# Performance work log

Hardware: AMD Instinct MI355X
Metric: run time of the kernel (lower is better)

The kernel has to match this reference:

```python
import jax, jax.numpy as jnp
import numpy as np

B, N, E = 4, 2048, 512
H, DK, DV = 8, 64, 64
QKV_OUT = H * (2 * DK + DV)  # 1536


def setup_inputs() -> dict:
    key = jax.random.key(0)
    ks = jax.random.split(key, 5)
    s_in = 1.0 / np.sqrt(E)
    s_o = 1.0 / np.sqrt(H * DV)
    x = jax.random.normal(ks[0], (B, N, E), dtype=jnp.float32)
    W_qkv = jax.random.uniform(ks[1], (E, QKV_OUT), jnp.float32, -s_in, s_in)
    b_qkv = jax.random.uniform(ks[2], (QKV_OUT,), jnp.float32, -s_in, s_in)
    W_o = jax.random.uniform(ks[3], (H * DV, E), jnp.float32, -s_o, s_o)
    b_o = jax.random.uniform(ks[4], (E,), jnp.float32, -s_o, s_o)
    return {"x": x, "W_qkv": W_qkv, "b_qkv": b_qkv, "W_o": W_o, "b_o": b_o}


def reference(x, W_qkv, b_qkv, W_o, b_o):
    scale = DK ** (-0.5)
    qkv = x @ W_qkv + b_qkv                      # [B, N, H*(2dk+dv)]
    # Faithful to torch: raw view (B, H, N, 2dk+dv), NOT a head-split transpose.
    qkv = qkv.reshape(B, H, N, 2 * DK + DV)
    q = qkv[..., :DK]
    k = qkv[..., DK:2 * DK]
    v = qkv[..., 2 * DK:]
    # Faithful bug: qk /= scale with scale = dk^-0.5 -> multiply by sqrt(dk).
    qk = jnp.einsum('bhnd,bhmd->bhnm', q, k) / scale   # [B, H, N, N]
    attn = jax.nn.softmax(qk, axis=-1)
    y = jnp.einsum('bhnm,bhmd->bhnd', attn, v)         # [B, H, N, dv]
    y = y.reshape(B, N, H * DV)
    return y @ W_o + b_o
```

## Files before the change

kernel.cpp:

```cpp
#include <hip/hip_runtime.h>
#include <hip/hip_bf16.h>
#include <math.h>


typedef __attribute__((ext_vector_type(8))) short bf16x8;
typedef __attribute__((ext_vector_type(4))) float f32x4;

#define MFMA16(a, b, c) __builtin_amdgcn_mfma_f32_16x16x32_bf16((a), (b), (c), 0, 0, 0)

__device__ __forceinline__ ushort f2bf_rne(float f) {
  union { float f; unsigned u; } v; v.f = f;
  return (ushort)((v.u + 0x7fffu + ((v.u >> 16) & 1u)) >> 16);
}
__device__ __forceinline__ float bf2f(ushort h) {
  union { float f; unsigned u; } v; v.u = ((unsigned)h) << 16; return v.f;
}
__device__ __forceinline__ void split2(float f, ushort& hi, ushort& lo) {
  union { float f; unsigned u; } v; v.f = f;
  hi = (ushort)(v.u >> 16);
  union { float f; unsigned u; } r; r.f = f - bf2f(hi);
  lo = (ushort)(r.u >> 16);
}

typedef __attribute__((address_space(3))) unsigned int lds_uint;
typedef const __attribute__((address_space(1))) unsigned int glob_uint;
__device__ __forceinline__ void gl_lds16(const ushort* g, short* l) {
  __builtin_amdgcn_global_load_lds((glob_uint*)g, (lds_uint*)l, 16, 0, 0);
}

template <bool ROOMY>
__global__ __launch_bounds__(256) void cvt_k(const float* __restrict__ wqkv,
                                             const float* __restrict__ wo,
                                             const float* __restrict__ x,
                                             ushort* __restrict__ wT_hi,
                                             ushort* __restrict__ wT_lo,
                                             ushort* __restrict__ woT,
                                             ushort* __restrict__ xh,
                                             ushort* __restrict__ xl)
{
  const int gid = blockIdx.x * 256 + threadIdx.x;
  if (gid < 786432) {
    const int c   = gid / 49152;
    const int rem = gid - c * 49152;
    const int n   = rem >> 5;
    const int k   = c * 32 + (rem & 31);
    ushort hi, lo; split2(wqkv[(size_t)k * 1536 + n], hi, lo);
    wT_hi[gid] = hi; wT_lo[gid] = lo;
  } else if (gid < 1048576) {
    const int g = gid - 786432;
    const int n = g >> 9, k = g & 511;
    woT[g] = f2bf_rne(wo[(size_t)k * 512 + n]);
  } else if (ROOMY) {
    const int g = gid - 1048576;
    float4 v = ((const float4*)x)[g];
    ushort4 hh, ll;
    split2(v.x, hh.x, ll.x); split2(v.y, hh.y, ll.y);
    split2(v.z, hh.z, ll.z); split2(v.w, hh.w, ll.w);
    ((ushort4*)xh)[g] = hh;
    ((ushort4*)xl)[g] = ll;
  }
}

template <bool PRECVT>
__global__ __launch_bounds__(256) void qkv_gemm_k(
    const float* __restrict__ x,
    const ushort* __restrict__ xh, const ushort* __restrict__ xl,
    const ushort* __restrict__ wT_hi, const ushort* __restrict__ wT_lo,
    const float* __restrict__ bqkv,
    ushort* __restrict__ q_hi, ushort* __restrict__ q_lo,
    ushort* __restrict__ k_hi, ushort* __restrict__ k_lo,
    ushort* __restrict__ v_nat)
{
  const int i = blockIdx.x, j = i >> 3;
  const int tmb = (i & 7) * 8 + (j & 7);
  const int tn  = j >> 3;
  const int tid = threadIdx.x, lane = tid & 63, w = tid >> 6;
  const int col16 = lane & 15, quad = lane >> 4;
  const int wr = w >> 1, wc = w & 1;

  __shared__ short sbuf[16384];

  const int wl   = w * 1024 + lane * 8;
  const int ldsw = w * 1024;
  const ushort* shp = wT_hi + (size_t)tn * 4096 + wl;
  const ushort* slp = wT_lo + (size_t)tn * 4096 + wl;

  const float*  axf[4];
  const ushort *axh[4], *axl[4];
#pragma unroll
  for (int rt = 0; rt < 4; ++rt) {
    const size_t rowoff = (size_t)(tmb * 128 + wr * 64 + rt * 16 + col16) * 512 + quad * 8;
    axf[rt] = x  + rowoff;
    axh[rt] = xh + rowoff;
    axl[rt] = xl + rowoff;
  }

  f32x4 acc[4][4];
#pragma unroll
  for (int rt = 0; rt < 4; ++rt)
#pragma unroll
    for (int ct = 0; ct < 4; ++ct) acc[rt][ct] = (f32x4){0.f, 0.f, 0.f, 0.f};

  gl_lds16(shp,       sbuf + ldsw);
  gl_lds16(shp + 512, sbuf + ldsw + 512);
  gl_lds16(slp,       sbuf + 8192 + ldsw);
  gl_lds16(slp + 512, sbuf + 8192 + ldsw + 512);
  __syncthreads();

  int buf = 0;
#pragma unroll
  for (int c = 0; c < 16; ++c) {
    if (c < 15) {
      const size_t co = (size_t)(c + 1) * 49152;
      const int nb = (buf ^ 1) * 4096;
      gl_lds16(shp + co,       sbuf + nb + ldsw);
      gl_lds16(shp + co + 512, sbuf + nb + ldsw + 512);
      gl_lds16(slp + co,       sbuf + 8192 + nb + ldsw);
      gl_lds16(slp + co + 512, sbuf + 8192 + nb + ldsw + 512);
    }
    const int k0 = c * 32;
    const short* bhb = sbuf + buf * 4096;
    const short* blb = sbuf + 8192 + buf * 4096;

    bf16x8 bh[4], bl[4];
#pragma unroll
    for (int ct = 0; ct < 4; ++ct) {
      const int roff = (wc * 64 + ct * 16 + col16) * 32 + quad * 8;
      bh[ct] = *(const bf16x8*)(bhb + roff);
      bl[ct] = *(const bf16x8*)(blb + roff);
    }
#pragma unroll
    for (int rt = 0; rt < 4; ++rt) {
      bf16x8 a_hi, a_lo;
      if constexpr (PRECVT) {
        a_hi = *(const bf16x8*)(axh[rt] + k0);
        a_lo = *(const bf16x8*)(axl[rt] + k0);
      } else {
        float4 xa = *(const float4*)(axf[rt] + k0);
        float4 xb = *(const float4*)(axf[rt] + k0 + 4);
#pragma unroll
        for (int jj = 0; jj < 4; ++jj) {
          ushort h, l;
          split2(((const float*)&xa)[jj], h, l);
          ((short*)&a_hi)[jj] = (short)h; ((short*)&a_lo)[jj] = (short)l;
          split2(((const float*)&xb)[jj], h, l);
          ((short*)&a_hi)[4 + jj] = (short)h; ((short*)&a_lo)[4 + jj] = (short)l;
        }
      }
#pragma unroll
      for (int ct = 0; ct < 4; ++ct) {
        acc[rt][ct] = MFMA16(a_hi, bh[ct], acc[rt][ct]);
        acc[rt][ct] = MFMA16(a_hi, bl[ct], acc[rt][ct]);
        acc[rt][ct] = MFMA16(a_lo, bh[ct], acc[rt][ct]);
      }
    }
    __syncthreads();
    buf ^= 1;
  }

  short* eph = sbuf + w * 2304;
  short* epl = eph + 1152;
  const int g0   = tn * 128 + wc * 64;
  const int sect = (g0 % 192) >> 6;
  const int s    = g0 / 192;
  float bv[4];
#pragma unroll
  for (int ct = 0; ct < 4; ++ct) bv[ct] = bqkv[g0 + ct * 16 + col16];

#pragma unroll
  for (int rt = 0; rt < 4; ++rt) {
#pragma unroll
    for (int ct = 0; ct < 4; ++ct) {
#pragma unroll
      for (int r = 0; r < 4; ++r) {
        const float val = acc[rt][ct][r] + bv[ct];
        const int o = (quad * 4 + r) * 72 + ct * 16 + col16;
        if (sect == 2) {
          eph[o] = (short)f2bf_rne(val);
        } else {
          ushort h, l; split2(val, h, l);
          eph[o] = (short)h; epl[o] = (short)l;
        }
      }
    }
#pragma unroll
    for (int p = 0; p < 2; ++p) {
      const int row = p * 8 + (lane >> 3);
      const int dsg = (lane & 7) * 8;
      const int grow = tmb * 128 + wr * 64 + rt * 16 + row;
      const int bhh = grow >> 8, a = grow & 255;
      const size_t idx = ((size_t)bhh * 2048 + 8 * a + s) * 64 + dsg;
      uint4 hv = *(const uint4*)(eph + row * 72 + dsg);
      if (sect == 0) {
        *(uint4*)(q_hi + idx) = hv;
        uint4 lv = *(const uint4*)(epl + row * 72 + dsg);
        *(uint4*)(q_lo + idx) = lv;
      } else if (sect == 1) {
        *(uint4*)(k_hi + idx) = hv;
        uint4 lv = *(const uint4*)(epl + row * 72 + dsg);
        *(uint4*)(k_lo + idx) = lv;
      } else {
        *(uint4*)(v_nat + idx) = hv;
      }
    }
  }
}

__global__ __launch_bounds__(256) void vtrans_k(const ushort* __restrict__ v_nat,
                                                ushort* __restrict__ vT)
{
  const int t  = blockIdx.x & 7;
  const int bh = blockIdx.x >> 3;
  const int tid = threadIdx.x;
  const int nl = tid & 63;
  const int dg = tid >> 6;
  const size_t base = (size_t)bh * 2048 * 64;
#pragma unroll
  for (int p = 0; p < 2; ++p) {
    const int dseg = dg + p * 4;
#pragma unroll
    for (int nb = 0; nb < 4; ++nb) {
      const int n = t * 256 + nb * 64 + nl;
      uint4 vv = *(const uint4*)(v_nat + base + (size_t)n * 64 + dseg * 8);
      const ushort* pv = (const ushort*)&vv;
#pragma unroll
      for (int j = 0; j < 8; ++j)
        vT[base + (size_t)(dseg * 8 + j) * 2048 + n] = pv[j];
    }
  }
}

__global__ __launch_bounds__(512, 4) void attn_k(
    const ushort* __restrict__ q_hi, const ushort* __restrict__ q_lo,
    const ushort* __restrict__ k_hi, const ushort* __restrict__ k_lo,
    const ushort* __restrict__ vT, ushort* __restrict__ y)
{
  const int i  = blockIdx.x;
  const int bh = (i & 7) * 4 + (i >> 7);
  const int qt = (i >> 3) & 15;
  const int tid = threadIdx.x, lane = tid & 63, w = tid >> 6;
  const int col16 = lane & 15, quad = lane >> 4;
  const int n7 = col16 & 7;

  __shared__ short sbuf[32768];

  const size_t base = (size_t)bh * 2048 * 64;
  const int qw = qt * 128 + w * 16;

  const ushort* khs = k_hi + base;
  const ushort* kls = k_lo + base;
  const ushort* vts = vT  + base;

  const int lrow = lane >> 3;
  const int lx8  = ((lane & 7) ^ lrow) * 8;

  bf16x8 qh[2], ql[2];
#pragma unroll
  for (int ks = 0; ks < 2; ++ks) {
    const size_t off = base + (size_t)(qw + col16) * 64 + ks * 32 + quad * 8;
    qh[ks] = *(const bf16x8*)(q_hi + off);
    ql[ks] = *(const bf16x8*)(q_lo + off);
  }

  f32x4 oacc[4];
#pragma unroll
  for (int ct = 0; ct < 4; ++ct) oacc[ct] = (f32x4){0.f, 0.f, 0.f, 0.f};
  f32x4 lsum = (f32x4){0.f, 0.f, 0.f, 0.f};

  const float S2 = 11.541560327111707f;

  short* wp0 = sbuf + 24576 + w * 1024;

#define STAGE_CHUNK(cnext, nb)                                                \
  {                                                                           \
    _Pragma("unroll")                                                         \
    for (int ii = 0; ii < 3; ++ii) {                                          \
      const int ins = w * 3 + ii;                                             \
      const int plane = ins >> 3, sub = ins & 7;                              \
      short* dst = sbuf + ((nb) * 3 + plane) * 4096 + sub * 512;              \
      const ushort* src;                                                      \
      if (plane == 2)                                                         \
        src = vts + (size_t)(sub * 8 + lrow) * 2048 + (cnext) * 64 + lx8;     \
      else                                                                    \
        src = (plane ? kls : khs) + (cnext) * 4096 + sub * 512 + lrow * 64 + lx8; \
      gl_lds16(src, dst);                                                     \
    }                                                                         \
  }

  STAGE_CHUNK(0, 0);
  __syncthreads();

  int buf = 0;
  for (int c = 0; c < 32; ++c) {
    if (c < 31) STAGE_CHUNK(c + 1, buf ^ 1);

    const short* kb = sbuf + (buf * 3) * 4096;
    const short* lb = kb + 4096;
    const short* vb = kb + 8192;

    f32x4 sacc[4];
#pragma unroll
    for (int ct = 0; ct < 4; ++ct) sacc[ct] = (f32x4){0.f, 0.f, 0.f, 0.f};

    __builtin_amdgcn_s_setprio(1);
#pragma unroll
    for (int ks = 0; ks < 2; ++ks) {
#pragma unroll
      for (int ct = 0; ct < 4; ++ct) {
        const int off = (ct * 16 + col16) * 64 + (((ks * 4 + quad) ^ n7) << 3);
        bf16x8 khf = *(const bf16x8*)(kb + off);
        bf16x8 klf = *(const bf16x8*)(lb + off);
        sacc[ct] = MFMA16(qh[ks], khf, sacc[ct]);
        sacc[ct] = MFMA16(qh[ks], klf, sacc[ct]);
        sacc[ct] = MFMA16(ql[ks], khf, sacc[ct]);
      }
    }
    __builtin_amdgcn_s_setprio(0);

#pragma unroll
    for (int ct = 0; ct < 4; ++ct) {
#pragma unroll
      for (int r = 0; r < 4; ++r) {
        const float p = __builtin_amdgcn_exp2f(fmaf(sacc[ct][r], S2, -128.0f));
        union { float f; unsigned u; } pu; pu.f = p;
        union { unsigned u; float f; } pb; pb.u = pu.u & 0xffff0000u;
        lsum[r] += pb.f;
        const int prow = quad * 4 + r;
        wp0[prow * 64 + ((ct * 16 + col16) ^ ((prow & 7) << 3))] =
            (short)(pu.u >> 16);
      }
    }

    __builtin_amdgcn_s_setprio(1);
#pragma unroll
    for (int ks = 0; ks < 2; ++ks) {
#pragma unroll
      for (int ct = 0; ct < 4; ++ct) {
        const int voff = (ct * 16 + col16) * 64 + (((ks * 4 + quad) ^ n7) << 3);
        bf16x8 vv = *(const bf16x8*)(vb + voff);
        const int poff = col16 * 64 + (((ks * 4 + quad) ^ n7) << 3);
        bf16x8 ap = *(const bf16x8*)(wp0 + poff);
        oacc[ct] = MFMA16(ap, vv, oacc[ct]);
      }
    }
    __builtin_amdgcn_s_setprio(0);

    __syncthreads();
    buf ^= 1;
  }

#pragma unroll
  for (int r = 0; r < 4; ++r) {
    float l = lsum[r];
#pragma unroll
    for (int off = 1; off < 16; off <<= 1) l += __shfl_xor(l, off, 64);
    const float inv = 1.f / l;
    const int n = qw + quad * 4 + r;
    const size_t orow = ((size_t)bh * 256 + (n >> 3)) * 512 + (n & 7) * 64;
#pragma unroll
    for (int ct = 0; ct < 4; ++ct)
      y[orow + ct * 16 + col16] = f2bf_rne(oacc[ct][r] * inv);
  }
#undef STAGE_CHUNK
}

__global__ __launch_bounds__(256) void out_gemm_k(
    const ushort* __restrict__ y, const ushort* __restrict__ woT,
    const float* __restrict__ bo, float* __restrict__ out)
{
  const int i = blockIdx.x, j = i >> 3;
  const int tmb = (i & 7) * 32 + (j & 31);
  const int tn  = j >> 5;
  const int tid = threadIdx.x, lane = tid & 63, w = tid >> 6;
  const int col16 = lane & 15, quad = lane >> 4;
  const int wr = w >> 1, wc = w & 1;

  __shared__ short b_lds[2][128][40];

  const int sn = tid >> 1, sk = (tid & 1) * 16;
  const ushort* bsrc = woT + (size_t)(tn * 128 + sn) * 512 + sk;

  const ushort* ay = y + (size_t)(tmb * 32 + wr * 16 + col16) * 512 + quad * 8;

  f32x4 acc[4];
#pragma unroll
  for (int ct = 0; ct < 4; ++ct) acc[ct] = (f32x4){0.f, 0.f, 0.f, 0.f};

  uint4 rb0 = *(const uint4*)(bsrc);
  uint4 rb1 = *(const uint4*)(bsrc + 8);
  *(uint4*)(&b_lds[0][sn][sk])     = rb0;
  *(uint4*)(&b_lds[0][sn][sk + 8]) = rb1;

  for (int c = 0; c < 16; ++c) {
    __syncthreads();
    if (c < 15) {
      const int k0 = (c + 1) * 32;
      rb0 = *(const uint4*)(bsrc + k0);
      rb1 = *(const uint4*)(bsrc + k0 + 8);
    }
    const int b = c & 1, k0 = c * 32;
    bf16x8 af = *(const bf16x8*)(ay + k0);
#pragma unroll
    for (int ct = 0; ct < 4; ++ct) {
      bf16x8 bfr = *(const bf16x8*)(&b_lds[b][wc * 64 + ct * 16 + col16][quad * 8]);
      acc[ct] = MFMA16(af, bfr, acc[ct]);
    }
    if (c < 15) {
      const int nb = b ^ 1;
      *(uint4*)(&b_lds[nb][sn][sk])     = rb0;
      *(uint4*)(&b_lds[nb][sn][sk + 8]) = rb1;
    }
  }
#pragma unroll
  for (int ct = 0; ct < 4; ++ct) {
    const int col = tn * 128 + wc * 64 + ct * 16 + col16;
    const float bval = bo[col];
#pragma unroll
    for (int r = 0; r < 4; ++r) {
      const int row = tmb * 32 + wr * 16 + quad * 4 + r;
      out[(size_t)row * 512 + col] = acc[ct][r] + bval;
    }
  }
}

extern "C" void kernel_launch(void* const* d_in, const int* in_sizes, int n_in,
                              void* d_out, int out_size, void* d_ws, size_t ws_size,
                              hipStream_t stream)
{
  const float* x    = (const float*)d_in[0];
  const float* Wqkv = (const float*)d_in[1];
  const float* bqkv = (const float*)d_in[2];
  const float* Wo   = (const float*)d_in[3];
  const float* bo   = (const float*)d_in[4];
  float* out = (float*)d_out;

  ushort* wT_hi = (ushort*)d_ws;
  ushort* wT_lo = wT_hi + 786432;
  ushort* woT   = wT_lo + 786432;
  ushort* q_hi  = woT   + 262144;
  ushort* q_lo  = q_hi  + 4194304;
  ushort* k_hi  = q_lo  + 4194304;
  ushort* k_lo  = k_hi  + 4194304;
  ushort* v_nat = k_lo  + 4194304;
  ushort* tail  = v_nat + 4194304;

  const bool roomy = ws_size >= 62390272ULL;
  ushort *xh, *xl, *vT, *y;
  if (roomy) {
    xh = tail; xl = tail + 4194304;
    vT = xh;   y  = xl;
  } else {
    xh = xl = nullptr;
    vT = tail; y = v_nat;
  }

  if (roomy) {
    cvt_k<true><<<8192, 256, 0, stream>>>(Wqkv, Wo, x, wT_hi, wT_lo, woT, xh, xl);
    qkv_gemm_k<true><<<768, 256, 0, stream>>>(x, xh, xl, wT_hi, wT_lo, bqkv,
                                              q_hi, q_lo, k_hi, k_lo, v_nat);
  } else {
    cvt_k<false><<<4096, 256, 0, stream>>>(Wqkv, Wo, x, wT_hi, wT_lo, woT,
                                           nullptr, nullptr);
    qkv_gemm_k<false><<<768, 256, 0, stream>>>(x, nullptr, nullptr, wT_hi, wT_lo,
                                               bqkv, q_hi, q_lo, k_hi, k_lo, v_nat);
  }
  vtrans_k<<<256, 256, 0, stream>>>(v_nat, vT);
  attn_k<<<512, 512, 0, stream>>>(q_hi, q_lo, k_hi, k_lo, vT, y);
  out_gemm_k<<<1024, 256, 0, stream>>>(y, woT, bo, out);
}
```

Measured before the change: 229.7 us.

## Transpose QK MFMA operands so P packs into vectorized LDS writes

```diff
diff --git a/kernel.cpp b/kernel.cpp
--- a/kernel.cpp
+++ b/kernel.cpp
@@ -265,7 +265,7 @@
   f32x4 oacc[4];
 #pragma unroll
   for (int ct = 0; ct < 4; ++ct) oacc[ct] = (f32x4){0.f, 0.f, 0.f, 0.f};
-  f32x4 lsum = (f32x4){0.f, 0.f, 0.f, 0.f};
+  float lsum = 0.f;
 
   const float S2 = 11.541560327111707f;
 
@@ -310,36 +310,37 @@
         const int off = (ct * 16 + col16) * 64 + (((ks * 4 + quad) ^ n7) << 3);
         bf16x8 khf = *(const bf16x8*)(kb + off);
         bf16x8 klf = *(const bf16x8*)(lb + off);
-        sacc[ct] = MFMA16(qh[ks], khf, sacc[ct]);
-        sacc[ct] = MFMA16(qh[ks], klf, sacc[ct]);
-        sacc[ct] = MFMA16(ql[ks], khf, sacc[ct]);
+        sacc[ct] = MFMA16(khf, qh[ks], sacc[ct]);
+        sacc[ct] = MFMA16(klf, qh[ks], sacc[ct]);
+        sacc[ct] = MFMA16(khf, ql[ks], sacc[ct]);
       }
     }
     __builtin_amdgcn_s_setprio(0);
 
 #pragma unroll
     for (int ct = 0; ct < 4; ++ct) {
-#pragma unroll
-      for (int r = 0; r < 4; ++r) {
-        const float p = __builtin_amdgcn_exp2f(fmaf(sacc[ct][r], S2, -128.0f));
-        union { float f; unsigned u; } pu; pu.f = p;
-        union { unsigned u; float f; } pb; pb.u = pu.u & 0xffff0000u;
-        lsum[r] += pb.f;
-        const int prow = quad * 4 + r;
-        wp0[prow * 64 + ((ct * 16 + col16) ^ ((prow & 7) << 3))] =
-            (short)(pu.u >> 16);
-      }
+      union { float f; unsigned u; } p0, p1, p2, p3;
+      p0.f = __builtin_amdgcn_exp2f(fmaf(sacc[ct][0], S2, -128.0f));
+      p1.f = __builtin_amdgcn_exp2f(fmaf(sacc[ct][1], S2, -128.0f));
+      p2.f = __builtin_amdgcn_exp2f(fmaf(sacc[ct][2], S2, -128.0f));
+      p3.f = __builtin_amdgcn_exp2f(fmaf(sacc[ct][3], S2, -128.0f));
+      lsum += (p0.f + p1.f) + (p2.f + p3.f);
+      const unsigned lo = (p0.u >> 16) | (p1.u & 0xffff0000u);
+      const unsigned hi = (p2.u >> 16) | (p3.u & 0xffff0000u);
+      const int g8 = (ct * 2 + (quad >> 1)) ^ n7;
+      uint2 pk; pk.x = lo; pk.y = hi;
+      *(uint2*)(wp0 + col16 * 64 + (g8 << 3) + ((quad & 1) << 2)) = pk;
     }
 
     __builtin_amdgcn_s_setprio(1);
 #pragma unroll
     for (int ks = 0; ks < 2; ++ks) {
+      bf16x8 ap = *(const bf16x8*)(wp0 + col16 * 64 +
+                                   (((ks * 4 + quad) ^ n7) << 3));
 #pragma unroll
       for (int ct = 0; ct < 4; ++ct) {
         const int voff = (ct * 16 + col16) * 64 + (((ks * 4 + quad) ^ n7) << 3);
         bf16x8 vv = *(const bf16x8*)(vb + voff);
-        const int poff = col16 * 64 + (((ks * 4 + quad) ^ n7) << 3);
-        bf16x8 ap = *(const bf16x8*)(wp0 + poff);
         oacc[ct] = MFMA16(ap, vv, oacc[ct]);
       }
     }
@@ -349,12 +350,11 @@
     buf ^= 1;
   }
 
+  lsum += __shfl_xor(lsum, 16, 64);
+  lsum += __shfl_xor(lsum, 32, 64);
 #pragma unroll
   for (int r = 0; r < 4; ++r) {
-    float l = lsum[r];
-#pragma unroll
-    for (int off = 1; off < 16; off <<= 1) l += __shfl_xor(l, off, 64);
-    const float inv = 1.f / l;
+    const float inv = 1.f / __shfl(lsum, quad * 4 + r, 64);
     const int n = qw + quad * 4 + r;
     const size_t orow = ((size_t)bh * 256 + (n >> 3)) * 512 + (n & 7) * 64;
 #pragma unroll
```

New measurement: 225.2 us. -2.0%, faster.
